# Performance work log

Hardware: AMD Instinct MI355X
Metric: run time of the kernel (lower is better)

## Reference

```python
import math
import jax
import jax.numpy as jnp
import numpy as np

B, N = 64, 64
R = N * (N - 1)
DIST_THRESH = 0.35


def _pair_indices(n):
    # edge e = i*(n-1) + j - (j > i): row-major over i, ascending j skipping j == i
    ii = np.repeat(np.arange(n), n - 1)
    jm = np.tile(np.arange(n), (n, 1))
    jj = jm[~np.eye(n, dtype=bool)].reshape(-1)
    return ii, jj


def _rot_basis(a):
    # a: [..., 1] angle -> [..., 2, 2] rotation basis rows [cos,sin],[cos(a+pi/2),sin(a+pi/2)]
    first = jnp.concatenate([jnp.cos(a), jnp.sin(a)], axis=-1)
    second = jnp.concatenate([jnp.cos(a + math.pi / 2), jnp.sin(a + math.pi / 2)], axis=-1)
    return jnp.stack([first, second], axis=-2)


def setup_inputs() -> dict:
    ks = jax.random.split(jax.random.key(0), 8)
    nrm = lambda k, shape, s=1.0: (jax.random.normal(k, shape) * s).astype(jnp.float32)
    return dict(
        objects_state=jax.random.uniform(ks[0], (B, N, 8), dtype=jnp.float32),
        objects_shape=nrm(ks[1], (B, N, 10)),
        relation_info=nrm(ks[2], (B, R, 3)),
        s_mean=jnp.zeros((8,), jnp.float32), s_std=jnp.ones((8,), jnp.float32),
        sh_mean=jnp.zeros((10,), jnp.float32), sh_std=jnp.ones((10,), jnp.float32),
        v_mean=jnp.zeros((3,), jnp.float32), v_std=jnp.ones((3,), jnp.float32),
        W1=nrm(ks[3], (32, 256), 32 ** -0.5), b1=jnp.zeros((256,), jnp.float32),
        W2=nrm(ks[4], (256, 128), 256 ** -0.5), b2=jnp.zeros((128,), jnp.float32),
        W3=nrm(ks[5], (141, 256), 141 ** -0.5), b3=jnp.zeros((256,), jnp.float32),
        W4=nrm(ks[6], (256, 3), 256 ** -0.5), b4=jnp.zeros((3,), jnp.float32),
    )


def reference(objects_state, objects_shape, relation_info, s_mean, s_std, sh_mean, sh_std,
              v_mean, v_std, W1, b1, W2, b2, W3, b3, W4, b4):
    n = objects_state.shape[1]
    ii, jj = _pair_indices(n)

    # ---- pre_proces: distance-threshold edge build into dense one-hot matrices ----
    pos = objects_state[:, :, 0:2]
    dist = jnp.sqrt(jnp.sum((pos[:, :, None, :] - pos[:, None, :, :]) ** 2, axis=-1))
    # torch: where(dist<0.35, dist, 0).nonzero() -> keeps dist<0.35 AND dist != 0 (drops self-edges)
    mask = ((dist < DIST_THRESH) & (dist != 0.0)).astype(jnp.float32)
    mask_flat = mask[:, ii, jj]  # [B, R]
    eye = jnp.eye(n, dtype=jnp.float32)
    receiver_relations = mask_flat[:, :, None] * eye[ii][None]  # [B, R, N]
    sender_relations = mask_flat[:, :, None] * eye[jj][None]    # [B, R, N]

    data_state = (objects_state - s_mean) / s_std
    data_shape = (objects_shape - sh_mean) / sh_std

    senders_state = jnp.einsum('brn,bnd->brd', sender_relations, data_state)
    receivers_state = jnp.einsum('brn,bnd->brd', receiver_relations, data_state)
    senders_shape = jnp.einsum('brn,bnd->brd', sender_relations, data_shape)
    receivers_shape = jnp.einsum('brn,bnd->brd', receiver_relations, data_shape)

    basis = _rot_basis(receivers_state[:, :, 2:3])  # [B, R, 2, 2]
    diff_state = senders_state - receivers_state
    temp = jnp.stack([diff_state[:, :, 0:2], diff_state[:, :, 3:5], senders_state[:, :, 6:8]], axis=-1)  # [B,R,2,3]
    tfed = jnp.einsum('brij,brjk->brik', basis, temp)  # [B,R,2,3]
    angle_diff = diff_state[:, :, 2:3]
    diff_feat = jnp.concatenate([
        tfed[:, :, :, 0], tfed[:, :, :, 1], tfed[:, :, :, 2],
        jnp.sin(2 * angle_diff), jnp.cos(2 * angle_diff),
        diff_state[:, :, 5:6],
    ], axis=-1)  # [B, R, 9]
    rel_data = jnp.concatenate([relation_info, diff_feat, receivers_shape, senders_shape], axis=-1)  # [B,R,32]

    obj_basis = _rot_basis(data_state[:, :, 2:3])  # [B, N, 2, 2]
    obj_vel_tfed = jnp.einsum('bnij,bnj->bni', obj_basis, data_state[:, :, 3:5])
    obj_data = jnp.concatenate([obj_vel_tfed, data_state[:, :, 5:6], data_shape], axis=-1)  # [B,N,13]

    # ---- interaction-network Net ----
    effects = jax.nn.relu(rel_data @ W1 + b1) @ W2 + b2  # [B, R, 128]
    agg = jnp.einsum('brn,bre->bne', receiver_relations, effects)  # [B, N, 128]
    out_vel = jax.nn.relu(jnp.concatenate([obj_data, agg], axis=-1) @ W3 + b3) @ W4 + b4  # [B,N,3]

    # ---- post_proces ----
    angles = objects_state[:, 1:, 2:3]
    pred = out_vel[:, 1:, :] * v_std + v_mean  # inv_transform_vel
    basis_back = _rot_basis(-angles)
    vel_back = jnp.einsum('bnij,bnj->bni', basis_back, pred[:, :, :2])
    x_dot = jnp.concatenate([vel_back, pred[:, :, 2:]], axis=-1)  # [B, N-1, 3]

    tp = np.eye(6, dtype=np.float32)
    tp[3:, 3:] = 0.0
    tq = np.zeros((3, 6), dtype=np.float32)
    for i in range(3):
        tq[i, i] = 1.0
        tq[i, 3 + i] = 1.0
    x_next = objects_state[:, 1:, :6] @ jnp.asarray(tp) + x_dot @ jnp.asarray(tq)
    return x_next  # [B, N-1, 6]
```

## Files before the change

kernel.cpp:

```cpp
#include <hip/hip_runtime.h>
#include <math.h>

#define BB 64
#define NN 64
#define NM1 63
#define RR (NN*(NN-1))

#define WS1_OFF 0
#define WS2_OFF 16384
#define WS3_OFF 81920
#define WSO_OFF 163840

typedef short bf16x8 __attribute__((ext_vector_type(8)));
typedef float f32x4 __attribute__((ext_vector_type(4)));
union U4 { uint4 u; bf16x8 b; };

__device__ inline unsigned int f2bf(float f) {
    unsigned int u = __float_as_uint(f);
    return (u + 0x7FFFu + ((u >> 16) & 1u)) >> 16;
}
__device__ inline unsigned int pack2(float a, float b) {
    return f2bf(a) | (f2bf(b) << 16);
}

__global__ __launch_bounds__(256) void prep_kernel(
    const float* __restrict__ objects_state,
    const float* __restrict__ objects_shape,
    const float* __restrict__ s_mean, const float* __restrict__ s_std,
    const float* __restrict__ sh_mean, const float* __restrict__ sh_std,
    const float* __restrict__ W1, const float* __restrict__ W2,
    const float* __restrict__ W3, unsigned char* __restrict__ ws)
{
    const int t = threadIdx.x;
    if (blockIdx.x < 40) {
        const int u = blockIdx.x*4 + (t >> 6), l = t & 63;
        const int col16 = l & 15, quad = l >> 4;
        float v[8];
        uint4* dst;
        if (u < 16) {
            const int nt = u, col = nt*16 + col16;
            #pragma unroll
            for (int j = 0; j < 8; ++j) {
                const int k = quad*8 + j;
                const int orig = k < 12 ? k : (k < 22 ? k+10 : k-10);
                v[j] = W1[orig*256 + col];
            }
            dst = (uint4*)(ws + WS1_OFF) + (nt*64 + l);
        } else if (u < 80) {
            const int w = u-16, nt = w >> 3, kc = w & 7, col = nt*16 + col16;
            #pragma unroll
            for (int j = 0; j < 8; ++j)
                v[j] = W2[(size_t)(kc*32 + quad*8 + j)*128 + col];
            dst = (uint4*)(ws + WS2_OFF) + ((nt*8 + kc)*64 + l);
        } else {
            const int w = u-80, nt = w/5, kc = w - nt*5, col = nt*16 + col16;
            #pragma unroll
            for (int j = 0; j < 8; ++j) {
                const int k = kc*32 + quad*8 + j;
                v[j] = (k < 141) ? W3[(size_t)k*256 + col] : 0.f;
            }
            dst = (uint4*)(ws + WS3_OFF) + ((nt*5 + kc)*64 + l);
        }
        uint4 o;
        o.x = pack2(v[0], v[1]); o.y = pack2(v[2], v[3]);
        o.z = pack2(v[4], v[5]); o.w = pack2(v[6], v[7]);
        *dst = o;
    } else {
        const int obj = (blockIdx.x - 40)*256 + t;
        float st[8], sh[10];
        #pragma unroll
        for (int c = 0; c < 8; ++c)  st[c] = objects_state[(size_t)obj*8 + c];
        #pragma unroll
        for (int c = 0; c < 10; ++c) sh[c] = objects_shape[(size_t)obj*10 + c];
        float f[28];
        f[0] = st[0]; f[1] = st[1]; f[26] = st[2]; f[27] = 0.f;
        #pragma unroll
        for (int c = 0; c < 8; ++c)  f[2+c]  = (st[c] - s_mean[c]) / s_std[c];
        #pragma unroll
        for (int c = 0; c < 10; ++c) f[10+c] = (sh[c] - sh_mean[c]) / sh_std[c];
        const float sa = sinf(f[4]), ca = cosf(f[4]);
        const float sr = sinf(st[2]), cr = cosf(st[2]);
        f[20] = ca; f[21] = sa; f[22] = cr; f[23] = sr;
        f[24] =  ca*f[5] + sa*f[6];
        f[25] = -sa*f[5] + ca*f[6];
        float4* dst = (float4*)(ws + WSO_OFF + (size_t)obj*112);
        #pragma unroll
        for (int q = 0; q < 7; ++q)
            dst[q] = make_float4(f[q*4], f[q*4+1], f[q*4+2], f[q*4+3]);
    }
}

__global__ __launch_bounds__(512) void main_kernel(
    const float* __restrict__ relation_info,
    const float* __restrict__ v_mean, const float* __restrict__ v_std,
    const float* __restrict__ b1, const float* __restrict__ b2,
    const float* __restrict__ b3,
    const float* __restrict__ W4, const float* __restrict__ b4,
    const unsigned char* __restrict__ ws,
    float* __restrict__ out)
{
    __shared__ __align__(16) float P[64][29];
    __shared__ __align__(16) unsigned int relb_w[8*64*16];
    __shared__ __align__(16) float RI[1512];
    __shared__ __align__(16) unsigned short s_h[16*264];
    __shared__ __align__(16) unsigned short s_q[16*168];
    __shared__ int   s_cntg[8];
    __shared__ float s_red[8][16][3];
    __shared__ float s_outv[16][3];

    const int b  = blockIdx.x >> 3;
    const int nb = (blockIdx.x & 7) * 8;
    const int t  = threadIdx.x;
    const int wv = t >> 6, lane = t & 63, col16 = lane & 15, quad = lane >> 4;

    float e_vs0=0.f,e_vs1=0.f,e_vs2=0.f,e_vm0=0.f,e_vm1=0.f,e_vm2=0.f,e_b4=0.f;
    if (t < 48) {
        e_vs0 = v_std[0]; e_vs1 = v_std[1]; e_vs2 = v_std[2];
        e_vm0 = v_mean[0]; e_vm1 = v_mean[1]; e_vm2 = v_mean[2];
        e_b4  = b4[t % 3];
    }

    {
        uint4 z = make_uint4(0,0,0,0);
        uint4* relb4 = (uint4*)relb_w;
        #pragma unroll
        for (int r = 0; r < 4; ++r) relb4[r*512 + t] = z;
        if (t < 336) ((uint4*)s_q)[t] = z;
        if (t < 8) s_cntg[t] = 0;
        if (t < 448) {
            const int obj = t / 7, q = t - obj*7;
            const float4 v = *(const float4*)(ws + WSO_OFF
                                + (size_t)(b*64 + obj)*112 + q*16);
            P[obj][q*4+0] = v.x; P[obj][q*4+1] = v.y;
            P[obj][q*4+2] = v.z; P[obj][q*4+3] = v.w;
        }
        const float* rsrc = relation_info + ((size_t)b*RR + nb*NM1)*3;
        #pragma unroll
        for (int r = 0; r < 3; ++r) {
            const int idx = r*512 + t;
            if (idx < 1512) RI[idx] = rsrc[idx];
        }
    }
    __syncthreads();

    if (t < 504) {
        const int g = t/63, k = t - g*63, n = nb + g, j = k + (k >= n);
        const float dx = P[n][0] - P[j][0];
        const float dy = P[n][1] - P[j][1];
        const float dist = sqrtf(dx*dx + dy*dy);
        if (dist < 0.35f && dist != 0.0f) {
            const int slot = atomicAdd(&s_cntg[g], 1);
            const int row = (g << 6) + slot;
            const int sw = (row >> 1) & 3;
            float f[32];
            f[0] = RI[t*3]; f[1] = RI[t*3+1]; f[2] = RI[t*3+2];
            const float rd0 = P[n][2], rd1 = P[n][3], rd2 = P[n][4],
                        rd3 = P[n][5], rd4 = P[n][6], rd5 = P[n][7];
            const float ca = P[n][20], sa = P[n][21];
            const float d0 = P[j][2]-rd0, d1 = P[j][3]-rd1, d2 = P[j][4]-rd2,
                        d3 = P[j][5]-rd3, d4 = P[j][6]-rd4, d5 = P[j][7]-rd5;
            f[3]  =  ca*d0 + sa*d1;
            f[4]  = -sa*d0 + ca*d1;
            f[5]  =  ca*d3 + sa*d4;
            f[6]  = -sa*d3 + ca*d4;
            f[7]  =  ca*P[j][8] + sa*P[j][9];
            f[8]  = -sa*P[j][8] + ca*P[j][9];
            f[9]  = sinf(2.f*d2);
            f[10] = cosf(2.f*d2);
            f[11] = d5;
            #pragma unroll
            for (int c = 0; c < 10; ++c) f[12+c] = P[j][10+c];
            #pragma unroll
            for (int c = 0; c < 10; ++c) f[22+c] = P[n][10+c];
            uint4* dst = (uint4*)&relb_w[row*16];
            #pragma unroll
            for (int w4 = 0; w4 < 4; ++w4) {
                uint4 o;
                o.x = pack2(f[w4*8+0], f[w4*8+1]);
                o.y = pack2(f[w4*8+2], f[w4*8+3]);
                o.z = pack2(f[w4*8+4], f[w4*8+5]);
                o.w = pack2(f[w4*8+6], f[w4*8+7]);
                dst[w4 ^ sw] = o;
            }
        }
    }
    __syncthreads();

    const int rd_sw = (quad ^ ((col16 >> 1) & 3)) * 4;

    {
        int cg[8];
        #pragma unroll
        for (int g = 0; g < 8; ++g) cg[g] = s_cntg[g];
        const uint4* w1f = (const uint4*)(ws + WS1_OFF);
        U4 bu0, bu1;
        bu0.u = w1f[(wv*2+0)*64 + lane];
        bu1.u = w1f[(wv*2+1)*64 + lane];
        const float b10 = b1[(wv*2+0)*16 + col16];
        const float b11 = b1[(wv*2+1)*16 + col16];
        float hs0[8], hs1[8];
        #pragma unroll
        for (int g = 0; g < 8; ++g) { hs0[g] = 0.f; hs1[g] = 0.f; }
        #pragma unroll
        for (int g = 0; g < 8; ++g) {
            const int mts = (cg[g] + 15) >> 4;
            for (int mt = 0; mt < mts; ++mt) {
                U4 au;
                au.u = *(const uint4*)&relb_w[((g<<6) + mt*16 + col16)*16 + rd_sw];
                f32x4 a0 = {0.f,0.f,0.f,0.f}, a1 = {0.f,0.f,0.f,0.f};
                a0 = __builtin_amdgcn_mfma_f32_16x16x32_bf16(au.b, bu0.b, a0, 0,0,0);
                a1 = __builtin_amdgcn_mfma_f32_16x16x32_bf16(au.b, bu1.b, a1, 0,0,0);
                #pragma unroll
                for (int i = 0; i < 4; ++i) {
                    hs0[g] += fmaxf(a0[i] + b10, 0.f);
                    hs1[g] += fmaxf(a1[i] + b11, 0.f);
                }
            }
        }
        const float rb0 = fmaxf(b10, 0.f), rb1 = fmaxf(b11, 0.f);
        #pragma unroll
        for (int g = 0; g < 8; ++g) {
            const int mts = (cg[g] + 15) >> 4;
            const float pad = (float)(mts*16 - cg[g]);
            float v0 = hs0[g], v1 = hs1[g];
            v0 += __shfl_xor(v0, 16); v0 += __shfl_xor(v0, 32);
            v1 += __shfl_xor(v1, 16); v1 += __shfl_xor(v1, 32);
            if (quad == 0) {
                s_h[g*264 + (wv*2+0)*16 + col16] =
                    (unsigned short)f2bf(v0 - pad*rb0);
                s_h[g*264 + (wv*2+1)*16 + col16] =
                    (unsigned short)f2bf(v1 - pad*rb1);
            }
        }
    }
    __syncthreads();

    if (t < 104) {
        const int m = t/13, c = t - m*13, n = nb + m;
        float v;
        if (c == 0) v = P[n][24];
        else if (c == 1) v = P[n][25];
        else if (c == 2) v = P[n][7];
        else v = P[n][10 + c - 3];
        s_q[m*168 + c] = (unsigned short)f2bf(v);
    }
    {
        U4 af[8];
        #pragma unroll
        for (int kc = 0; kc < 8; ++kc)
            af[kc].u = *(const uint4*)&s_h[(lane & 15)*264 + kc*32 + quad*8];
        float cntv[4];
        #pragma unroll
        for (int i = 0; i < 4; ++i)
            cntv[i] = (float)s_cntg[(quad*4 + i) & 7];
        const uint4* w2f = (const uint4*)(ws + WS2_OFF);
        f32x4 acc = {0.f,0.f,0.f,0.f};
        #pragma unroll
        for (int kc = 0; kc < 8; ++kc) {
            U4 bu; bu.u = w2f[(wv*8 + kc)*64 + lane];
            acc = __builtin_amdgcn_mfma_f32_16x16x32_bf16(af[kc].b, bu.b, acc, 0,0,0);
        }
        const float b2v = b2[wv*16 + col16];
        #pragma unroll
        for (int i = 0; i < 4; ++i) {
            const int row = quad*4 + i;
            s_q[row*168 + 13 + wv*16 + col16] =
                (unsigned short)f2bf(acc[i] + cntv[i]*b2v);
        }
    }
    __syncthreads();

    {
        U4 af3[5];
        #pragma unroll
        for (int kc = 0; kc < 5; ++kc)
            af3[kc].u = *(const uint4*)&s_q[(lane & 15)*168 + kc*32 + quad*8];
        const uint4* w3f = (const uint4*)(ws + WS3_OFF);
        float p[4][3];
        #pragma unroll
        for (int i = 0; i < 4; ++i) { p[i][0]=0.f; p[i][1]=0.f; p[i][2]=0.f; }
        #pragma unroll
        for (int ntl = 0; ntl < 2; ++ntl) {
            const int nt = wv + ntl*8, col = nt*16 + col16;
            f32x4 acc = {0.f,0.f,0.f,0.f};
            #pragma unroll
            for (int kc = 0; kc < 5; ++kc) {
                U4 bu; bu.u = w3f[(nt*5 + kc)*64 + lane];
                acc = __builtin_amdgcn_mfma_f32_16x16x32_bf16(af3[kc].b, bu.b, acc, 0,0,0);
            }
            const float b3v = b3[col];
            const float w40 = W4[col*3+0], w41 = W4[col*3+1], w42 = W4[col*3+2];
            #pragma unroll
            for (int i = 0; i < 4; ++i) {
                const float h = fmaxf(acc[i] + b3v, 0.f);
                p[i][0] = fmaf(h, w40, p[i][0]);
                p[i][1] = fmaf(h, w41, p[i][1]);
                p[i][2] = fmaf(h, w42, p[i][2]);
            }
        }
        #pragma unroll
        for (int off = 1; off < 16; off <<= 1)
            #pragma unroll
            for (int i = 0; i < 4; ++i) {
                p[i][0] += __shfl_xor(p[i][0], off);
                p[i][1] += __shfl_xor(p[i][1], off);
                p[i][2] += __shfl_xor(p[i][2], off);
            }
        if (col16 == 0)
            #pragma unroll
            for (int i = 0; i < 4; ++i) {
                s_red[wv][quad*4+i][0] = p[i][0];
                s_red[wv][quad*4+i][1] = p[i][1];
                s_red[wv][quad*4+i][2] = p[i][2];
            }
    }
    __syncthreads();
    if (t < 48) {
        const int m = t/3, o = t - m*3;
        float acc = e_b4;
        #pragma unroll
        for (int w = 0; w < 8; ++w) acc += s_red[w][m][o];
        s_outv[m][o] = acc;
    }
    __syncthreads();

    if (t < 48) {
        const int m = t/6, i = t - m*6, n = nb + m;
        if (n >= 1) {
            const float q0 = s_outv[m][0]*e_vs0 + e_vm0;
            const float q1 = s_outv[m][1]*e_vs1 + e_vm1;
            const float q2 = s_outv[m][2]*e_vs2 + e_vm2;
            const float cr = P[n][22], sr = P[n][23];
            const float xd0 = cr*q0 - sr*q1;
            const float xd1 = sr*q0 + cr*q1;
            const int im = i % 3;
            const float xd = (im == 0) ? xd0 : (im == 1) ? xd1 : q2;
            float base = 0.f;
            if (i == 0) base = P[n][0];
            else if (i == 1) base = P[n][1];
            else if (i == 2) base = P[n][26];
            out[((size_t)b*NM1 + (n-1))*6 + i] = base + xd;
        }
    }
}

extern "C" void kernel_launch(void* const* d_in, const int* in_sizes, int n_in,
                              void* d_out, int out_size, void* d_ws, size_t ws_size,
                              hipStream_t stream) {
    const float* objects_state = (const float*)d_in[0];
    const float* objects_shape = (const float*)d_in[1];
    const float* relation_info = (const float*)d_in[2];
    const float* s_mean  = (const float*)d_in[3];
    const float* s_std   = (const float*)d_in[4];
    const float* sh_mean = (const float*)d_in[5];
    const float* sh_std  = (const float*)d_in[6];
    const float* v_mean  = (const float*)d_in[7];
    const float* v_std   = (const float*)d_in[8];
    const float* W1 = (const float*)d_in[9];
    const float* b1 = (const float*)d_in[10];
    const float* W2 = (const float*)d_in[11];
    const float* b2 = (const float*)d_in[12];
    const float* W3 = (const float*)d_in[13];
    const float* b3 = (const float*)d_in[14];
    const float* W4 = (const float*)d_in[15];
    const float* b4 = (const float*)d_in[16];
    unsigned char* ws = (unsigned char*)d_ws;

    prep_kernel<<<dim3(56), dim3(256), 0, stream>>>(
        objects_state, objects_shape, s_mean, s_std, sh_mean, sh_std,
        W1, W2, W3, ws);
    main_kernel<<<dim3(BB*8), dim3(512), 0, stream>>>(
        relation_info, v_mean, v_std, b1, b2, b3, W4, b4,
        ws, (float*)d_out);
}
```

Measured before the change: 104.8 us.

## Fuse per-object preprocessing into main kernel and compact edges with wave ballot

Per-object normalization and trig features move from the prep kernel into the main kernel, where 64 threads compute them straight into shared memory, so the workspace round-trip goes away and prep shrinks to weight packing. Edge compaction uses one wave per receiver with ballot/popcount instead of shared atomics. Relation info is loaded directly into registers rather than staged in LDS, and W1 fragments and biases are loaded early to overlap with setup. The cost is that each of the 8 blocks per batch now recomputes the same 64 objects' features, including sin/cos, redundantly.

```diff
diff --git a/kernel.cpp b/kernel.cpp
--- a/kernel.cpp
+++ b/kernel.cpp
@@ -9,7 +9,6 @@
 #define WS1_OFF 0
 #define WS2_OFF 16384
 #define WS3_OFF 81920
-#define WSO_OFF 163840
 
 typedef short bf16x8 __attribute__((ext_vector_type(8)));
 typedef float f32x4 __attribute__((ext_vector_type(4)));
@@ -24,74 +23,50 @@
 }
 
 __global__ __launch_bounds__(256) void prep_kernel(
-    const float* __restrict__ objects_state,
-    const float* __restrict__ objects_shape,
-    const float* __restrict__ s_mean, const float* __restrict__ s_std,
-    const float* __restrict__ sh_mean, const float* __restrict__ sh_std,
     const float* __restrict__ W1, const float* __restrict__ W2,
     const float* __restrict__ W3, unsigned char* __restrict__ ws)
 {
     const int t = threadIdx.x;
-    if (blockIdx.x < 40) {
-        const int u = blockIdx.x*4 + (t >> 6), l = t & 63;
-        const int col16 = l & 15, quad = l >> 4;
-        float v[8];
-        uint4* dst;
-        if (u < 16) {
-            const int nt = u, col = nt*16 + col16;
-            #pragma unroll
-            for (int j = 0; j < 8; ++j) {
-                const int k = quad*8 + j;
-                const int orig = k < 12 ? k : (k < 22 ? k+10 : k-10);
-                v[j] = W1[orig*256 + col];
-            }
-            dst = (uint4*)(ws + WS1_OFF) + (nt*64 + l);
-        } else if (u < 80) {
-            const int w = u-16, nt = w >> 3, kc = w & 7, col = nt*16 + col16;
-            #pragma unroll
-            for (int j = 0; j < 8; ++j)
-                v[j] = W2[(size_t)(kc*32 + quad*8 + j)*128 + col];
-            dst = (uint4*)(ws + WS2_OFF) + ((nt*8 + kc)*64 + l);
-        } else {
-            const int w = u-80, nt = w/5, kc = w - nt*5, col = nt*16 + col16;
-            #pragma unroll
-            for (int j = 0; j < 8; ++j) {
-                const int k = kc*32 + quad*8 + j;
-                v[j] = (k < 141) ? W3[(size_t)k*256 + col] : 0.f;
-            }
-            dst = (uint4*)(ws + WS3_OFF) + ((nt*5 + kc)*64 + l);
-        }
-        uint4 o;
-        o.x = pack2(v[0], v[1]); o.y = pack2(v[2], v[3]);
-        o.z = pack2(v[4], v[5]); o.w = pack2(v[6], v[7]);
-        *dst = o;
+    const int u = blockIdx.x*4 + (t >> 6), l = t & 63;
+    const int col16 = l & 15, quad = l >> 4;
+    float v[8];
+    uint4* dst;
+    if (u < 16) {
+        const int nt = u, col = nt*16 + col16;
+        #pragma unroll
+        for (int j = 0; j < 8; ++j) {
+            const int k = quad*8 + j;
+            const int orig = k < 12 ? k : (k < 22 ? k+10 : k-10);
+            v[j] = W1[orig*256 + col];
+        }
+        dst = (uint4*)(ws + WS1_OFF) + (nt*64 + l);
+    } else if (u < 80) {
+        const int w = u-16, nt = w >> 3, kc = w & 7, col = nt*16 + col16;
+        #pragma unroll
+        for (int j = 0; j < 8; ++j)
+            v[j] = W2[(size_t)(kc*32 + quad*8 + j)*128 + col];
+        dst = (uint4*)(ws + WS2_OFF) + ((nt*8 + kc)*64 + l);
     } else {
-        const int obj = (blockIdx.x - 40)*256 + t;
-        float st[8], sh[10];
-        #pragma unroll
-        for (int c = 0; c < 8; ++c)  st[c] = objects_state[(size_t)obj*8 + c];
-        #pragma unroll
-        for (int c = 0; c < 10; ++c) sh[c] = objects_shape[(size_t)obj*10 + c];
-        float f[28];
-        f[0] = st[0]; f[1] = st[1]; f[26] = st[2]; f[27] = 0.f;
-        #pragma unroll
-        for (int c = 0; c < 8; ++c)  f[2+c]  = (st[c] - s_mean[c]) / s_std[c];
-        #pragma unroll
-        for (int c = 0; c < 10; ++c) f[10+c] = (sh[c] - sh_mean[c]) / sh_std[c];
-        const float sa = sinf(f[4]), ca = cosf(f[4]);
-        const float sr = sinf(st[2]), cr = cosf(st[2]);
-        f[20] = ca; f[21] = sa; f[22] = cr; f[23] = sr;
-        f[24] =  ca*f[5] + sa*f[6];
-        f[25] = -sa*f[5] + ca*f[6];
-        float4* dst = (float4*)(ws + WSO_OFF + (size_t)obj*112);
-        #pragma unroll
-        for (int q = 0; q < 7; ++q)
-            dst[q] = make_float4(f[q*4], f[q*4+1], f[q*4+2], f[q*4+3]);
-    }
+        const int w = u-80, nt = w/5, kc = w - nt*5, col = nt*16 + col16;
+        #pragma unroll
+        for (int j = 0; j < 8; ++j) {
+            const int k = kc*32 + quad*8 + j;
+            v[j] = (k < 141) ? W3[(size_t)k*256 + col] : 0.f;
+        }
+        dst = (uint4*)(ws + WS3_OFF) + ((nt*5 + kc)*64 + l);
+    }
+    uint4 o;
+    o.x = pack2(v[0], v[1]); o.y = pack2(v[2], v[3]);
+    o.z = pack2(v[4], v[5]); o.w = pack2(v[6], v[7]);
+    *dst = o;
 }
 
 __global__ __launch_bounds__(512) void main_kernel(
+    const float* __restrict__ objects_state,
+    const float* __restrict__ objects_shape,
     const float* __restrict__ relation_info,
+    const float* __restrict__ s_mean, const float* __restrict__ s_std,
+    const float* __restrict__ sh_mean, const float* __restrict__ sh_std,
     const float* __restrict__ v_mean, const float* __restrict__ v_std,
     const float* __restrict__ b1, const float* __restrict__ b2,
     const float* __restrict__ b3,
@@ -101,7 +76,6 @@
 {
     __shared__ __align__(16) float P[64][29];
     __shared__ __align__(16) unsigned int relb_w[8*64*16];
-    __shared__ __align__(16) float RI[1512];
     __shared__ __align__(16) unsigned short s_h[16*264];
     __shared__ __align__(16) unsigned short s_q[16*168];
     __shared__ int   s_cntg[8];
@@ -113,6 +87,22 @@
     const int t  = threadIdx.x;
     const int wv = t >> 6, lane = t & 63, col16 = lane & 15, quad = lane >> 4;
 
+    U4 bu0, bu1;
+    {
+        const uint4* w1f = (const uint4*)(ws + WS1_OFF);
+        bu0.u = w1f[(wv*2+0)*64 + lane];
+        bu1.u = w1f[(wv*2+1)*64 + lane];
+    }
+    const float b10 = b1[(wv*2+0)*16 + col16];
+    const float b11 = b1[(wv*2+1)*16 + col16];
+
+    float ri0 = 0.f, ri1 = 0.f, ri2 = 0.f;
+    if (lane < 63) {
+        const float* rp = relation_info
+            + ((size_t)b*RR + (size_t)(nb + wv)*NM1 + lane)*3;
+        ri0 = rp[0]; ri1 = rp[1]; ri2 = rp[2];
+    }
+
     float e_vs0=0.f,e_vs1=0.f,e_vs2=0.f,e_vm0=0.f,e_vm1=0.f,e_vm2=0.f,e_b4=0.f;
     if (t < 48) {
         e_vs0 = v_std[0]; e_vs1 = v_std[1]; e_vs2 = v_std[2];
@@ -126,39 +116,58 @@
         #pragma unroll
         for (int r = 0; r < 4; ++r) relb4[r*512 + t] = z;
         if (t < 336) ((uint4*)s_q)[t] = z;
-        if (t < 8) s_cntg[t] = 0;
-        if (t < 448) {
-            const int obj = t / 7, q = t - obj*7;
-            const float4 v = *(const float4*)(ws + WSO_OFF
-                                + (size_t)(b*64 + obj)*112 + q*16);
-            P[obj][q*4+0] = v.x; P[obj][q*4+1] = v.y;
-            P[obj][q*4+2] = v.z; P[obj][q*4+3] = v.w;
-        }
-        const float* rsrc = relation_info + ((size_t)b*RR + nb*NM1)*3;
-        #pragma unroll
-        for (int r = 0; r < 3; ++r) {
-            const int idx = r*512 + t;
-            if (idx < 1512) RI[idx] = rsrc[idx];
-        }
-    }
-    __syncthreads();
-
-    if (t < 504) {
-        const int g = t/63, k = t - g*63, n = nb + g, j = k + (k >= n);
-        const float dx = P[n][0] - P[j][0];
-        const float dy = P[n][1] - P[j][1];
-        const float dist = sqrtf(dx*dx + dy*dy);
-        if (dist < 0.35f && dist != 0.0f) {
-            const int slot = atomicAdd(&s_cntg[g], 1);
+        if (t < 64) {
+            const int n = b*64 + t;
+            const float4* sp4 = (const float4*)(objects_state + (size_t)n*8);
+            const float4 sA = sp4[0], sB = sp4[1];
+            float st[8] = {sA.x, sA.y, sA.z, sA.w, sB.x, sB.y, sB.z, sB.w};
+            const float2* hp2 = (const float2*)(objects_shape + (size_t)n*10);
+            float sh[10];
+            #pragma unroll
+            for (int c = 0; c < 5; ++c) {
+                const float2 v = hp2[c];
+                sh[c*2] = v.x; sh[c*2+1] = v.y;
+            }
+            float f[28];
+            f[0] = st[0]; f[1] = st[1]; f[26] = st[2]; f[27] = 0.f;
+            #pragma unroll
+            for (int c = 0; c < 8; ++c)  f[2+c]  = (st[c] - s_mean[c]) / s_std[c];
+            #pragma unroll
+            for (int c = 0; c < 10; ++c) f[10+c] = (sh[c] - sh_mean[c]) / sh_std[c];
+            const float sa = sinf(f[4]), ca = cosf(f[4]);
+            const float sr = sinf(st[2]), cr = cosf(st[2]);
+            f[20] = ca; f[21] = sa; f[22] = cr; f[23] = sr;
+            f[24] =  ca*f[5] + sa*f[6];
+            f[25] = -sa*f[5] + ca*f[6];
+            #pragma unroll
+            for (int c = 0; c < 28; ++c) P[t][c] = f[c];
+        }
+    }
+    __syncthreads();
+
+    {
+        const int g = wv, n = nb + g;
+        bool pred = false;
+        int j = 0;
+        if (lane < 63) {
+            j = lane + (lane >= n);
+            const float dx = P[n][0] - P[j][0];
+            const float dy = P[n][1] - P[j][1];
+            const float dist = sqrtf(dx*dx + dy*dy);
+            pred = (dist < 0.35f) && (dist != 0.0f);
+        }
+        const unsigned long long mask = __ballot(pred);
+        if (lane == 0) s_cntg[g] = __popcll(mask);
+        if (pred) {
+            const int slot = __popcll(mask & ((1ull << lane) - 1ull));
             const int row = (g << 6) + slot;
             const int sw = (row >> 1) & 3;
             float f[32];
-            f[0] = RI[t*3]; f[1] = RI[t*3+1]; f[2] = RI[t*3+2];
-            const float rd0 = P[n][2], rd1 = P[n][3], rd2 = P[n][4],
-                        rd3 = P[n][5], rd4 = P[n][6], rd5 = P[n][7];
+            f[0] = ri0; f[1] = ri1; f[2] = ri2;
             const float ca = P[n][20], sa = P[n][21];
-            const float d0 = P[j][2]-rd0, d1 = P[j][3]-rd1, d2 = P[j][4]-rd2,
-                        d3 = P[j][5]-rd3, d4 = P[j][6]-rd4, d5 = P[j][7]-rd5;
+            const float d0 = P[j][2]-P[n][2], d1 = P[j][3]-P[n][3];
+            const float d2 = P[j][4]-P[n][4], d3 = P[j][5]-P[n][5];
+            const float d4 = P[j][6]-P[n][6], d5 = P[j][7]-P[n][7];
             f[3]  =  ca*d0 + sa*d1;
             f[4]  = -sa*d0 + ca*d1;
             f[5]  =  ca*d3 + sa*d4;
@@ -192,12 +201,6 @@
         int cg[8];
         #pragma unroll
         for (int g = 0; g < 8; ++g) cg[g] = s_cntg[g];
-        const uint4* w1f = (const uint4*)(ws + WS1_OFF);
-        U4 bu0, bu1;
-        bu0.u = w1f[(wv*2+0)*64 + lane];
-        bu1.u = w1f[(wv*2+1)*64 + lane];
-        const float b10 = b1[(wv*2+0)*16 + col16];
-        const float b11 = b1[(wv*2+1)*16 + col16];
         float hs0[8], hs1[8];
         #pragma unroll
         for (int g = 0; g < 8; ++g) { hs0[g] = 0.f; hs1[g] = 0.f; }
@@ -366,10 +369,9 @@
     const float* b4 = (const float*)d_in[16];
     unsigned char* ws = (unsigned char*)d_ws;
 
-    prep_kernel<<<dim3(56), dim3(256), 0, stream>>>(
-        objects_state, objects_shape, s_mean, s_std, sh_mean, sh_std,
-        W1, W2, W3, ws);
+    prep_kernel<<<dim3(40), dim3(256), 0, stream>>>(W1, W2, W3, ws);
     main_kernel<<<dim3(BB*8), dim3(512), 0, stream>>>(
-        relation_info, v_mean, v_std, b1, b2, b3, W4, b4,
-        ws, (float*)d_out);
-}
+        objects_state, objects_shape, relation_info,
+        s_mean, s_std, sh_mean, sh_std, v_mean, v_std,
+        b1, b2, b3, W4, b4, ws, (float*)d_out);
+}
```

Result: no change. 104.3 us, median of 2 (-0.5%).
